# Kernel optimization log

Hardware: AMD Instinct MI355X
Metric: run time of the kernel (lower is better)

The kernel has to match this reference:

```python
import jax, jax.numpy as jnp
import numpy as np

N, D, H, DH, DFF, E = 4096, 512, 8, 64, 2048, 65536


def setup_inputs() -> dict:
    key = jax.random.key(0)
    ks = jax.random.split(key, 20)
    g = lambda k, s: jax.random.normal(k, s, dtype=jnp.float32) * 0.02
    inp = {
        'x': jax.random.normal(ks[0], (N, D), dtype=jnp.float32),
        'edge_index': jax.random.randint(ks[1], (2, E), 0, N),
        'edge_attr': jax.random.uniform(ks[2], (E,), dtype=jnp.float32),
        'Wg': g(ks[3], (D, D)), 'bg': jnp.zeros((D,), jnp.float32),
        'ln1_s': jnp.ones((D,), jnp.float32), 'ln1_b': jnp.zeros((D,), jnp.float32),
        'Wq': g(ks[4], (D, D)), 'bq': jnp.zeros((D,), jnp.float32),
        'Wk': g(ks[5], (D, D)), 'bk': jnp.zeros((D,), jnp.float32),
        'Wv': g(ks[6], (D, D)), 'bv': jnp.zeros((D,), jnp.float32),
        'Wo': g(ks[7], (D, D)), 'bo': jnp.zeros((D,), jnp.float32),
        'ln2_s': jnp.ones((D,), jnp.float32), 'ln2_b': jnp.zeros((D,), jnp.float32),
        'W1': g(ks[8], (D, DFF)), 'b1': jnp.zeros((DFF,), jnp.float32),
        'W2': g(ks[9], (DFF, D)), 'b2': jnp.zeros((D,), jnp.float32),
        'Wa': g(ks[10], (2 * D, D)), 'ba': jnp.zeros((D,), jnp.float32),
    }
    return inp


def _ln(x, s, b):
    m = x.mean(-1, keepdims=True)
    v = ((x - m) ** 2).mean(-1, keepdims=True)
    return (x - m) * jax.lax.rsqrt(v + 1e-5) * s + b


def _gcn(x, edge_index, ew, Wg, bg):
    # GCNConv: linear, add self-loops (weight 1), sym deg normalization, scatter-add
    xt = x @ Wg                                   # [N, D]
    src = jnp.concatenate([edge_index[0], jnp.arange(N)])
    dst = jnp.concatenate([edge_index[1], jnp.arange(N)])
    w = jnp.concatenate([ew, jnp.ones((N,), ew.dtype)])
    deg = jax.ops.segment_sum(w, dst, num_segments=N)
    dinv = jnp.where(deg > 0, jax.lax.rsqrt(jnp.maximum(deg, 1e-12)), 0.0)
    coef = dinv[src] * w * dinv[dst]              # [E+N]
    out = jax.ops.segment_sum(xt[src] * coef[:, None], dst, num_segments=N)
    return out + bg


def _tfm(x, p):
    # pre-LN vanilla transformer block over all N nodes as one sequence
    h = _ln(x, p['ln1_s'], p['ln1_b'])
    q = (h @ p['Wq'] + p['bq']).reshape(N, H, DH)
    k = (h @ p['Wk'] + p['bk']).reshape(N, H, DH)
    v = (h @ p['Wv'] + p['bv']).reshape(N, H, DH)
    scores = jnp.einsum('nhd,mhd->hnm', q, k) / np.sqrt(DH)
    a = jax.nn.softmax(scores, axis=-1)
    o = jnp.einsum('hnm,mhd->nhd', a, v).reshape(N, D)
    x = x + o @ p['Wo'] + p['bo']
    h2 = _ln(x, p['ln2_s'], p['ln2_b'])
    mlp = jax.nn.gelu(h2 @ p['W1'] + p['b1']) @ p['W2'] + p['b2']
    return x + mlp


def reference(x, edge_index, edge_attr, Wg, bg, ln1_s, ln1_b, Wq, bq, Wk, bk, Wv, bv,
              Wo, bo, ln2_s, ln2_b, W1, b1, W2, b2, Wa, ba):
    p = dict(ln1_s=ln1_s, ln1_b=ln1_b, Wq=Wq, bq=bq, Wk=Wk, bk=bk, Wv=Wv, bv=bv,
             Wo=Wo, bo=bo, ln2_s=ln2_s, ln2_b=ln2_b, W1=W1, b1=b1, W2=W2, b2=b2)
    mp = _gcn(x, edge_index, edge_attr, Wg, bg)
    tf = _tfm(x, p)
    return x + jnp.concatenate([mp, tf], axis=-1) @ Wa + ba
```

## Files before the change

### kernel.cpp

```cpp
#include <hip/hip_runtime.h>
#include <math.h>

#define N_NODES 4096
#define DMODEL  512
#define NHEAD   8
#define DHEAD   64
#define DFF     2048
#define NEDGE   65536
#define QKVLD   1536

typedef unsigned short u16;
typedef __bf16 bf16x8 __attribute__((ext_vector_type(8)));
typedef float  f32x4  __attribute__((ext_vector_type(4)));
typedef short  s16x4  __attribute__((ext_vector_type(4)));

#if defined(__has_builtin)
#if __has_builtin(__builtin_amdgcn_mfma_f32_16x16x16bf16_1k)
#define HAS_MFMA_1K 1
#endif
#endif

__device__ inline f32x4 mfma16(bf16x8 a, bf16x8 b, f32x4 c) {
    return __builtin_amdgcn_mfma_f32_16x16x32_bf16(a, b, c, 0, 0, 0);
}

#ifdef HAS_MFMA_1K
__device__ inline f32x4 mfma1k(s16x4 a, s16x4 b, f32x4 c) {
    return __builtin_amdgcn_mfma_f32_16x16x16bf16_1k(a, b, c, 0, 0, 0);
}
__device__ inline s16x4 pack_bf4(f32x4 p) {
    union { float f; unsigned u; } a0, a1, a2, a3;
    a0.f = p[0]; a1.f = p[1]; a2.f = p[2]; a3.f = p[3];
    unsigned lo = __builtin_amdgcn_perm(a1.u + 0x8000u, a0.u + 0x8000u, 0x07060302u);
    unsigned hi = __builtin_amdgcn_perm(a3.u + 0x8000u, a2.u + 0x8000u, 0x07060302u);
    union { unsigned u[2]; s16x4 v; } r;
    r.u[0] = lo; r.u[1] = hi;
    return r.v;
}
#endif

__device__ inline u16 f2bf(float f) {
    union { float f; unsigned u; } v; v.f = f;
    unsigned r = v.u + 0x7fff + ((v.u >> 16) & 1);
    return (u16)(r >> 16);
}

__device__ inline float bf2f(u16 v) {
    union { unsigned u; float f; } t; t.u = ((unsigned)v) << 16; return t.f;
}

__device__ inline float gelu_tanh(float x) {
    float x3 = x * x * x;
    float t = tanhf(0.7978845608028654f * (x + 0.044715f * x3));
    return 0.5f * x * (1.0f + t);
}

#define GBM 128
#define GBN 128
#define GBK 32
#define GP  40

template <int ACT, int OBF16>
__launch_bounds__(256)
__global__ void mfma_gemm(const u16* __restrict__ A, const u16* __restrict__ Bt,
                          const float* __restrict__ bias, const float* __restrict__ res,
                          void* __restrict__ Cout, int M, int Nn, int K, float scale,
                          int ldC, int ldRes) {
    __shared__ u16 Asm[2][GBM * GP];
    __shared__ u16 Bsm[2][GBN * GP];

    const int tid = threadIdx.x;
    const int w = tid >> 6;
    const int lane = tid & 63;
    const int quad = lane >> 4;
    const int l15 = lane & 15;
    const int row0 = blockIdx.y * GBM;
    const int col0 = blockIdx.x * GBN;
    const int wm = (w & 1) * 64;
    const int wn = (w >> 1) * 64;

    f32x4 acc[4][4];
#pragma unroll
    for (int i = 0; i < 4; ++i)
#pragma unroll
        for (int j = 0; j < 4; ++j) acc[i][j] = (f32x4){0.f, 0.f, 0.f, 0.f};

    const int c1 = tid, c2 = tid + 256;
    const int ar1 = c1 >> 2, ak1 = (c1 & 3) * 8;
    const int ar2 = c2 >> 2, ak2 = (c2 & 3) * 8;

    {
        uint4 a0 = *(const uint4*)&A [(size_t)(row0 + ar1) * K + ak1];
        uint4 a1 = *(const uint4*)&A [(size_t)(row0 + ar2) * K + ak2];
        uint4 b0 = *(const uint4*)&Bt[(size_t)(col0 + ar1) * K + ak1];
        uint4 b1 = *(const uint4*)&Bt[(size_t)(col0 + ar2) * K + ak2];
        *(uint4*)&Asm[0][ar1 * GP + ak1] = a0;
        *(uint4*)&Asm[0][ar2 * GP + ak2] = a1;
        *(uint4*)&Bsm[0][ar1 * GP + ak1] = b0;
        *(uint4*)&Bsm[0][ar2 * GP + ak2] = b1;
    }
    __syncthreads();

    const int nT = K / GBK;
    for (int t = 0; t < nT; ++t) {
        const int buf = t & 1;
        uint4 an0, an1, bn0, bn1;
        if (t + 1 < nT) {
            const int k0 = (t + 1) * GBK;
            an0 = *(const uint4*)&A [(size_t)(row0 + ar1) * K + k0 + ak1];
            an1 = *(const uint4*)&A [(size_t)(row0 + ar2) * K + k0 + ak2];
            bn0 = *(const uint4*)&Bt[(size_t)(col0 + ar1) * K + k0 + ak1];
            bn1 = *(const uint4*)&Bt[(size_t)(col0 + ar2) * K + k0 + ak2];
        }
        bf16x8 af[4], bf[4];
#pragma unroll
        for (int i = 0; i < 4; ++i) {
            af[i] = *(const bf16x8*)&Asm[buf][(wm + i * 16 + l15) * GP + quad * 8];
            bf[i] = *(const bf16x8*)&Bsm[buf][(wn + i * 16 + l15) * GP + quad * 8];
        }
#pragma unroll
        for (int i = 0; i < 4; ++i)
#pragma unroll
            for (int j = 0; j < 4; ++j)
                acc[i][j] = mfma16(af[i], bf[j], acc[i][j]);
        if (t + 1 < nT) {
            *(uint4*)&Asm[buf ^ 1][ar1 * GP + ak1] = an0;
            *(uint4*)&Asm[buf ^ 1][ar2 * GP + ak2] = an1;
            *(uint4*)&Bsm[buf ^ 1][ar1 * GP + ak1] = bn0;
            *(uint4*)&Bsm[buf ^ 1][ar2 * GP + ak2] = bn1;
            __syncthreads();
        }
    }

#pragma unroll
    for (int j = 0; j < 4; ++j) {
        const int col = col0 + wn + j * 16 + l15;
        const float bc = bias ? bias[col] : 0.f;
#pragma unroll
        for (int i = 0; i < 4; ++i) {
#pragma unroll
            for (int r = 0; r < 4; ++r) {
                const int row = row0 + wm + i * 16 + quad * 4 + r;
                float o = (acc[i][j][r] + bc) * scale;
                if (ACT == 1) o = gelu_tanh(o);
                if (res) o += res[(size_t)row * ldRes + col];
                if (OBF16)
                    ((u16*)Cout)[(size_t)row * ldC + col] = f2bf(o);
                else
                    ((float*)Cout)[(size_t)row * ldC + col] = o;
            }
        }
    }
}

template <int ACT, int OBF16>
__launch_bounds__(256)
__global__ void mfma_gemm64(const u16* __restrict__ A, const u16* __restrict__ Bt,
                            const float* __restrict__ bias, const float* __restrict__ res,
                            void* __restrict__ Cout, int M, int Nn, int K, float scale,
                            int ldC, int ldRes) {
    __shared__ u16 Asm[2][64 * GP];
    __shared__ u16 Bsm[2][128 * GP];

    const int tid = threadIdx.x;
    const int w = tid >> 6;
    const int lane = tid & 63;
    const int quad = lane >> 4;
    const int l15 = lane & 15;
    const int row0 = blockIdx.y * 64;
    const int col0 = blockIdx.x * GBN;
    const int wn = w * 32;

    f32x4 acc[4][2];
#pragma unroll
    for (int i = 0; i < 4; ++i)
#pragma unroll
        for (int j = 0; j < 2; ++j) acc[i][j] = (f32x4){0.f, 0.f, 0.f, 0.f};

    const int c1 = tid, c2 = tid + 256;
    const int ar1 = c1 >> 2, ak1 = (c1 & 3) * 8;
    const int ar2 = c2 >> 2, ak2 = (c2 & 3) * 8;

    {
        uint4 a0 = *(const uint4*)&A [(size_t)(row0 + ar1) * K + ak1];
        uint4 b0 = *(const uint4*)&Bt[(size_t)(col0 + ar1) * K + ak1];
        uint4 b1 = *(const uint4*)&Bt[(size_t)(col0 + ar2) * K + ak2];
        *(uint4*)&Asm[0][ar1 * GP + ak1] = a0;
        *(uint4*)&Bsm[0][ar1 * GP + ak1] = b0;
        *(uint4*)&Bsm[0][ar2 * GP + ak2] = b1;
    }
    __syncthreads();

    const int nT = K / GBK;
    for (int t = 0; t < nT; ++t) {
        const int buf = t & 1;
        uint4 an, bn0, bn1;
        if (t + 1 < nT) {
            const int k0 = (t + 1) * GBK;
            an  = *(const uint4*)&A [(size_t)(row0 + ar1) * K + k0 + ak1];
            bn0 = *(const uint4*)&Bt[(size_t)(col0 + ar1) * K + k0 + ak1];
            bn1 = *(const uint4*)&Bt[(size_t)(col0 + ar2) * K + k0 + ak2];
        }
        bf16x8 af[4], bf[2];
#pragma unroll
        for (int i = 0; i < 4; ++i)
            af[i] = *(const bf16x8*)&Asm[buf][(i * 16 + l15) * GP + quad * 8];
#pragma unroll
        for (int j = 0; j < 2; ++j)
            bf[j] = *(const bf16x8*)&Bsm[buf][(wn + j * 16 + l15) * GP + quad * 8];
#pragma unroll
        for (int i = 0; i < 4; ++i)
#pragma unroll
            for (int j = 0; j < 2; ++j)
                acc[i][j] = mfma16(af[i], bf[j], acc[i][j]);
        if (t + 1 < nT) {
            *(uint4*)&Asm[buf ^ 1][ar1 * GP + ak1] = an;
            *(uint4*)&Bsm[buf ^ 1][ar1 * GP + ak1] = bn0;
            *(uint4*)&Bsm[buf ^ 1][ar2 * GP + ak2] = bn1;
            __syncthreads();
        }
    }

#pragma unroll
    for (int j = 0; j < 2; ++j) {
        const int col = col0 + wn + j * 16 + l15;
        const float bc = bias ? bias[col] : 0.f;
#pragma unroll
        for (int i = 0; i < 4; ++i) {
#pragma unroll
            for (int r = 0; r < 4; ++r) {
                const int row = row0 + i * 16 + quad * 4 + r;
                float o = (acc[i][j][r] + bc) * scale;
                if (ACT == 1) o = gelu_tanh(o);
                if (res) o += res[(size_t)row * ldRes + col];
                if (OBF16)
                    ((u16*)Cout)[(size_t)row * ldC + col] = f2bf(o);
                else
                    ((float*)Cout)[(size_t)row * ldC + col] = o;
            }
        }
    }
}

__launch_bounds__(256)
__global__ void qkvg_gemm(const u16* __restrict__ xb, const u16* __restrict__ hb,
                          const u16* __restrict__ Wall,
                          const float* __restrict__ bq, const float* __restrict__ bk,
                          const float* __restrict__ bv,
                          u16* __restrict__ xtb, u16* __restrict__ qkvb) {
    __shared__ u16 Asm[2][64 * GP];
    __shared__ u16 Bsm[2][128 * GP];

    const int tid = threadIdx.x;
    const int w = tid >> 6;
    const int lane = tid & 63;
    const int quad = lane >> 4;
    const int l15 = lane & 15;
    const int row0 = blockIdx.y * 64;
    const int col0 = blockIdx.x * GBN;
    const int wn = w * 32;
    const int K = DMODEL;
    const u16* A = (col0 < 512) ? xb : hb;

    f32x4 acc[4][2];
#pragma unroll
    for (int i = 0; i < 4; ++i)
#pragma unroll
        for (int j = 0; j < 2; ++j) acc[i][j] = (f32x4){0.f, 0.f, 0.f, 0.f};

    const int c1 = tid, c2 = tid + 256;
    const int ar1 = c1 >> 2, ak1 = (c1 & 3) * 8;
    const int ar2 = c2 >> 2, ak2 = (c2 & 3) * 8;

    {
        uint4 a0 = *(const uint4*)&A   [(size_t)(row0 + ar1) * K + ak1];
        uint4 b0 = *(const uint4*)&Wall[(size_t)(col0 + ar1) * K + ak1];
        uint4 b1 = *(const uint4*)&Wall[(size_t)(col0 + ar2) * K + ak2];
        *(uint4*)&Asm[0][ar1 * GP + ak1] = a0;
        *(uint4*)&Bsm[0][ar1 * GP + ak1] = b0;
        *(uint4*)&Bsm[0][ar2 * GP + ak2] = b1;
    }
    __syncthreads();

    const int nT = K / GBK;
    for (int t = 0; t < nT; ++t) {
        const int buf = t & 1;
        uint4 an, bn0, bn1;
        if (t + 1 < nT) {
            const int k0 = (t + 1) * GBK;
            an  = *(const uint4*)&A   [(size_t)(row0 + ar1) * K + k0 + ak1];
            bn0 = *(const uint4*)&Wall[(size_t)(col0 + ar1) * K + k0 + ak1];
            bn1 = *(const uint4*)&Wall[(size_t)(col0 + ar2) * K + k0 + ak2];
        }
        bf16x8 af[4], bf[2];
#pragma unroll
        for (int i = 0; i < 4; ++i)
            af[i] = *(const bf16x8*)&Asm[buf][(i * 16 + l15) * GP + quad * 8];
#pragma unroll
        for (int j = 0; j < 2; ++j)
            bf[j] = *(const bf16x8*)&Bsm[buf][(wn + j * 16 + l15) * GP + quad * 8];
#pragma unroll
        for (int i = 0; i < 4; ++i)
#pragma unroll
            for (int j = 0; j < 2; ++j)
                acc[i][j] = mfma16(af[i], bf[j], acc[i][j]);
        if (t + 1 < nT) {
            *(uint4*)&Asm[buf ^ 1][ar1 * GP + ak1] = an;
            *(uint4*)&Bsm[buf ^ 1][ar1 * GP + ak1] = bn0;
            *(uint4*)&Bsm[buf ^ 1][ar2 * GP + ak2] = bn1;
            __syncthreads();
        }
    }

#pragma unroll
    for (int j = 0; j < 2; ++j) {
        const int col = col0 + wn + j * 16 + l15;
        float bc = 0.f, scale = 1.f;
        if (col >= 512 && col < 1024) { bc = bq[col - 512]; scale = 0.125f; }
        else if (col >= 1024 && col < 1536) bc = bk[col - 1024];
        else if (col >= 1536) bc = bv[col - 1536];
#pragma unroll
        for (int i = 0; i < 4; ++i) {
#pragma unroll
            for (int r = 0; r < 4; ++r) {
                const int row = row0 + i * 16 + quad * 4 + r;
                const u16 ob = f2bf((acc[i][j][r] + bc) * scale);
                if (col < 512)
                    xtb[(size_t)row * 512 + col] = ob;
                else
                    qkvb[(size_t)row * QKVLD + col - 512] = ob;
            }
        }
    }
}

__launch_bounds__(256)
__global__ void wtrans_all_kernel(
    const float* __restrict__ Wg, const float* __restrict__ Wq,
    const float* __restrict__ Wk, const float* __restrict__ Wv,
    const float* __restrict__ Wo, const float* __restrict__ W1,
    const float* __restrict__ W2, const float* __restrict__ Wa,
    u16* __restrict__ Wgt, u16* __restrict__ Wqt, u16* __restrict__ Wkt,
    u16* __restrict__ Wvt, u16* __restrict__ Wot, u16* __restrict__ W1t,
    u16* __restrict__ W2t, u16* __restrict__ Wat) {
    __shared__ u16 t[32][34];
    const int id = blockIdx.x;
    const float* W; u16* Wt; int K, Nn, bx, by;
    if (id < 1280) {
        const int m = id >> 8, tt = id & 255;
        bx = tt & 15; by = tt >> 4; K = 512; Nn = 512;
        W  = (m == 0) ? Wg  : (m == 1) ? Wq  : (m == 2) ? Wk  : (m == 3) ? Wv  : Wo;
        Wt = (m == 0) ? Wgt : (m == 1) ? Wqt : (m == 2) ? Wkt : (m == 3) ? Wvt : Wot;
    } else if (id < 2304) {
        const int tt = id - 1280; bx = tt & 63; by = tt >> 6;
        K = 512; Nn = 2048; W = W1; Wt = W1t;
    } else if (id < 3328) {
        const int tt = id - 2304; bx = tt & 15; by = tt >> 4;
        K = 2048; Nn = 512; W = W2; Wt = W2t;
    } else {
        const int tt = id - 3328; bx = tt & 15; by = tt >> 4;
        K = 1024; Nn = 512; W = Wa; Wt = Wat;
    }
    const int k0 = by * 32, n0 = bx * 32;
    const int r = threadIdx.x >> 3, c4 = (threadIdx.x & 7) * 4;
    float4 v = *(const float4*)&W[(size_t)(k0 + r) * Nn + n0 + c4];
    t[r][c4 + 0] = f2bf(v.x); t[r][c4 + 1] = f2bf(v.y);
    t[r][c4 + 2] = f2bf(v.z); t[r][c4 + 3] = f2bf(v.w);
    __syncthreads();
    u16 tmp[4];
#pragma unroll
    for (int i = 0; i < 4; ++i) tmp[i] = t[c4 + i][r];
    u16* op = Wt + (size_t)(n0 + r) * K + k0 + c4;
    *(uint2*)op = *(uint2*)tmp;
}

__global__ void cvt_bf16_kernel(const float* __restrict__ in, u16* __restrict__ out) {
    size_t i = ((size_t)blockIdx.x * 256 + threadIdx.x) * 4;
    float4 v = *(const float4*)&in[i];
    ushort4 o;
    o.x = f2bf(v.x); o.y = f2bf(v.y); o.z = f2bf(v.z); o.w = f2bf(v.w);
    *(ushort4*)&out[i] = o;
}

__device__ inline float block_sum_256(float v, float* red4) {
#pragma unroll
    for (int o = 32; o > 0; o >>= 1) v += __shfl_down(v, o, 64);
    const int lane = threadIdx.x & 63;
    const int w = threadIdx.x >> 6;
    if (lane == 0) red4[w] = v;
    __syncthreads();
    return red4[0] + red4[1] + red4[2] + red4[3];
}

__launch_bounds__(256)
__global__ void ln_kernel(const float* __restrict__ X, const float* __restrict__ s,
                          const float* __restrict__ b, u16* __restrict__ Y) {
    __shared__ float redA[4];
    __shared__ float redB[4];
    const int row = blockIdx.x;
    const int tid = threadIdx.x;
    const float* xr = X + (size_t)row * DMODEL;
    float v0 = xr[tid], v1 = xr[tid + 256];
    float total = block_sum_256(v0 + v1, redA);
    float mean = total * (1.0f / DMODEL);
    float d0 = v0 - mean, d1 = v1 - mean;
    float sq = block_sum_256(d0 * d0 + d1 * d1, redB);
    float inv = rsqrtf(sq * (1.0f / DMODEL) + 1e-5f);
    Y[(size_t)row * DMODEL + tid] = f2bf(d0 * inv * s[tid] + b[tid]);
    Y[(size_t)row * DMODEL + tid + 256] = f2bf(d1 * inv * s[tid + 256] + b[tid + 256]);
}

__global__ void gcn_prep_kernel(float* __restrict__ deg, int* __restrict__ cnt) {
    int i = blockIdx.x * 256 + threadIdx.x;
    deg[i] = 1.0f;
    cnt[i] = 0;
}

__global__ void gcn_count_kernel(const int* __restrict__ ei, const float* __restrict__ ew,
                                 float* __restrict__ deg, int* __restrict__ cnt) {
    int e = blockIdx.x * 256 + threadIdx.x;
    int d = ei[NEDGE + e];
    atomicAdd(&cnt[d], 1);
    atomicAdd(&deg[d], ew[e]);
}

__global__ void dinv_kernel(const float* __restrict__ deg, float* __restrict__ dinv) {
    int i = blockIdx.x * 256 + threadIdx.x;
    float d = deg[i];
    dinv[i] = (d > 0.f) ? rsqrtf(fmaxf(d, 1e-12f)) : 0.f;
}

__launch_bounds__(256)
__global__ void gcn_prefix_kernel(const int* __restrict__ cnt, int* __restrict__ off,
                                  int* __restrict__ cur) {
    __shared__ int part[256];
    const int tid = threadIdx.x;
    int local[16];
    int s = 0;
#pragma unroll
    for (int i = 0; i < 16; ++i) { local[i] = s; s += cnt[tid * 16 + i]; }
    part[tid] = s;
    __syncthreads();
    if (tid == 0) {
        int run = 0;
        for (int j = 0; j < 256; ++j) { int t = part[j]; part[j] = run; run += t; }
        off[N_NODES] = run;
    }
    __syncthreads();
    int p = part[tid];
#pragma unroll
    for (int i = 0; i < 16; ++i) {
        off[tid * 16 + i] = p + local[i];
        cur[tid * 16 + i] = p + local[i];
    }
}

__global__ void gcn_fill_kernel(const int* __restrict__ ei, const float* __restrict__ ew,
                                int* __restrict__ cur, int* __restrict__ esrc,
                                float* __restrict__ eww) {
    int e = blockIdx.x * 256 + threadIdx.x;
    int s = ei[e], d = ei[NEDGE + e];
    int pos = atomicAdd(&cur[d], 1);
    esrc[pos] = s;
    eww[pos] = ew[e];
}

__launch_bounds__(256)
__global__ void gcn_gather_kernel(const u16* __restrict__ xtb, const int* __restrict__ off,
                                  const int* __restrict__ esrc, const float* __restrict__ eww,
                                  const float* __restrict__ dinv, const float* __restrict__ bg,
                                  u16* __restrict__ catb) {
    const int d = blockIdx.x;
    const int b0 = off[d], b1 = off[d + 1];
    const float did = dinv[d];
    const int c = threadIdx.x * 2;
    float a0 = 0.f, a1 = 0.f;
    for (int j = b0; j < b1; ++j) {
        const int s = esrc[j];
        const float coef = dinv[s] * eww[j] * did;
        const unsigned pv = *(const unsigned*)&xtb[(size_t)s * DMODEL + c];
        a0 += coef * bf2f((u16)(pv & 0xffff));
        a1 += coef * bf2f((u16)(pv >> 16));
    }
    {
        const unsigned pv = *(const unsigned*)&xtb[(size_t)d * DMODEL + c];
        const float sl = did * did;
        a0 += sl * bf2f((u16)(pv & 0xffff));
        a1 += sl * bf2f((u16)(pv >> 16));
    }
    const unsigned pk = (unsigned)f2bf(a0 + bg[c]) | ((unsigned)f2bf(a1 + bg[c + 1]) << 16);
    *(unsigned*)&catb[(size_t)d * 1024 + c] = pk;
}

__launch_bounds__(256)
__global__ void vtrans_kernel(const u16* __restrict__ Qkv, u16* __restrict__ Vt) {
    __shared__ u16 t[64][72];
    const int h = blockIdx.x, n0 = blockIdx.y * 64;
    const int r = threadIdx.x >> 2, cg = (threadIdx.x & 3) * 16;
    const uint4* vp = (const uint4*)(Qkv + (size_t)(n0 + r) * QKVLD + 1024 + h * DHEAD + cg);
    *(uint4*)&t[r][cg] = vp[0];
    *(uint4*)&t[r][cg + 8] = vp[1];
    __syncthreads();
    const int d = threadIdx.x >> 2;
    u16 tmp[16];
#pragma unroll
    for (int i = 0; i < 16; ++i) tmp[i] = t[cg + i][d];
    u16* op = Vt + ((size_t)h * DHEAD + d) * N_NODES + n0 + cg;
    *(uint4*)&op[0] = *(uint4*)&tmp[0];
    *(uint4*)&op[8] = *(uint4*)&tmp[8];
}

#define TK 64
#define AP 88
#define NSPLIT 4
#define KSPAN (N_NODES / NSPLIT)

__launch_bounds__(128)
__global__ void attn_kernel(const u16* __restrict__ Qkv, const u16* __restrict__ Vtb,
                            float* __restrict__ Op0, float* __restrict__ Op1,
                            float* __restrict__ Op2, float* __restrict__ Op3,
                            float* __restrict__ lpart) {
    __shared__ u16 Ks[64 * AP];
    __shared__ u16 Vs[64 * AP];
#ifndef HAS_MFMA_1K
    __shared__ u16 Ps[2][2][16 * AP];
#endif

    const int h = blockIdx.x;
    const int q0 = blockIdx.y * 64;
    const int sp = blockIdx.z;
    float* __restrict__ Opx = (sp == 0) ? Op0 : (sp == 1) ? Op1 : (sp == 2) ? Op2 : Op3;
    const int kbase = sp * KSPAN;

    const int tid = threadIdx.x;
    const int w = tid >> 6;
    const int lane = tid & 63;
    const int quad = lane >> 4;
    const int l15 = lane & 15;

    const u16* qp = Qkv + (size_t)(q0 + w * 32 + l15) * QKVLD + h * DHEAD + quad * 8;
    bf16x8 qf[2][2];
    qf[0][0] = *(const bf16x8*)qp;
    qf[0][1] = *(const bf16x8*)(qp + 32);
    qf[1][0] = *(const bf16x8*)(qp + 16 * QKVLD);
    qf[1][1] = *(const bf16x8*)(qp + 16 * QKVLD + 32);

    f32x4 Oa[2][4];
#pragma unroll
    for (int a = 0; a < 2; ++a)
#pragma unroll
        for (int g = 0; g < 4; ++g) Oa[a][g] = (f32x4){0.f, 0.f, 0.f, 0.f};
    float ls[2] = {0.f, 0.f};

    const int sr = tid >> 1, sc = (tid & 1) * 32;

    for (int kt = kbase; kt < kbase + KSPAN; kt += TK) {
        {
            const uint4* kg = (const uint4*)(Qkv + (size_t)(kt + sr) * QKVLD + 512 + h * DHEAD + sc);
            uint4* kd = (uint4*)&Ks[sr * AP + sc];
            kd[0] = kg[0]; kd[1] = kg[1]; kd[2] = kg[2]; kd[3] = kg[3];
            const uint4* vg = (const uint4*)(Vtb + ((size_t)h * DHEAD + sr) * N_NODES + kt + sc);
            uint4* vd = (uint4*)&Vs[sr * AP + sc];
            vd[0] = vg[0]; vd[1] = vg[1]; vd[2] = vg[2]; vd[3] = vg[3];
        }
        __syncthreads();

        f32x4 St[2][4];
#pragma unroll
        for (int f = 0; f < 4; ++f) {
            const u16* kr = &Ks[(f * 16 + l15) * AP + quad * 8];
            bf16x8 k0 = *(const bf16x8*)kr;
            bf16x8 k1 = *(const bf16x8*)(kr + 32);
#pragma unroll
            for (int a = 0; a < 2; ++a) {
                f32x4 z = (f32x4){0.f, 0.f, 0.f, 0.f};
                z = mfma16(k0, qf[a][0], z);
                St[a][f] = mfma16(k1, qf[a][1], z);
            }
        }

#ifdef HAS_MFMA_1K
        s16x4 pk[2][4];
#pragma unroll
        for (int a = 0; a < 2; ++a)
#pragma unroll
            for (int f = 0; f < 4; ++f) {
                f32x4 p;
                p[0] = __expf(St[a][f][0]);
                p[1] = __expf(St[a][f][1]);
                p[2] = __expf(St[a][f][2]);
                p[3] = __expf(St[a][f][3]);
                ls[a] += (p[0] + p[1]) + (p[2] + p[3]);
                pk[a][f] = pack_bf4(p);
            }
#pragma unroll
        for (int f = 0; f < 4; ++f)
#pragma unroll
            for (int g = 0; g < 4; ++g) {
                const s16x4 vv = *(const s16x4*)&Vs[(g * 16 + l15) * AP + f * 16 + quad * 4];
                Oa[0][g] = mfma1k(pk[0][f], vv, Oa[0][g]);
                Oa[1][g] = mfma1k(pk[1][f], vv, Oa[1][g]);
            }
#else
        bf16x8 pa[2][2];
#pragma unroll
        for (int a = 0; a < 2; ++a) {
            u16* pw = Ps[w][a];
#pragma unroll
            for (int f = 0; f < 4; ++f) {
                float p0 = __expf(St[a][f][0]);
                float p1 = __expf(St[a][f][1]);
                float p2 = __expf(St[a][f][2]);
                float p3 = __expf(St[a][f][3]);
                ls[a] += (p0 + p1) + (p2 + p3);
                ushort4 pkk;
                pkk.x = f2bf(p0); pkk.y = f2bf(p1); pkk.z = f2bf(p2); pkk.w = f2bf(p3);
                *(uint2*)&pw[l15 * AP + f * 16 + quad * 4] = *(uint2*)&pkk;
            }
            const u16* pr = &pw[l15 * AP + quad * 8];
            pa[a][0] = *(const bf16x8*)pr;
            pa[a][1] = *(const bf16x8*)(pr + 32);
        }
#pragma unroll
        for (int g = 0; g < 4; ++g) {
            const u16* vr = &Vs[(g * 16 + l15) * AP + quad * 8];
            bf16x8 v0 = *(const bf16x8*)vr;
            bf16x8 v1 = *(const bf16x8*)(vr + 32);
#pragma unroll
            for (int a = 0; a < 2; ++a) {
                Oa[a][g] = mfma16(pa[a][0], v0, Oa[a][g]);
                Oa[a][g] = mfma16(pa[a][1], v1, Oa[a][g]);
            }
        }
#endif
        __syncthreads();
    }

#pragma unroll
    for (int a = 0; a < 2; ++a) {
        float s = ls[a];
        s += __shfl_xor(s, 16, 64);
        s += __shfl_xor(s, 32, 64);
        const int rowbase = q0 + w * 32 + a * 16;
        if (quad == 0)
            lpart[(size_t)(sp * NHEAD + h) * N_NODES + rowbase + l15] = s;
#pragma unroll
        for (int r = 0; r < 4; ++r) {
            float* op = Opx + (size_t)(rowbase + quad * 4 + r) * DMODEL + h * DHEAD + l15;
#pragma unroll
            for (int g = 0; g < 4; ++g) op[g * 16] = Oa[a][g][r];
        }
    }
}

__global__ void attn_reduce_kernel(const float* __restrict__ Op0, const float* __restrict__ Op1,
                                   const float* __restrict__ Op2, const float* __restrict__ Op3,
                                   const float* __restrict__ lpart, u16* __restrict__ attb) {
    size_t i4 = ((size_t)blockIdx.x * 256 + threadIdx.x) * 4;
    const int row = (int)(i4 >> 9);
    const int h = ((int)i4 & 511) >> 6;
    float4 o0 = *(const float4*)&Op0[i4];
    float4 o1 = *(const float4*)&Op1[i4];
    float4 o2 = *(const float4*)&Op2[i4];
    float4 o3 = *(const float4*)&Op3[i4];
    const float* lp = lpart + (size_t)h * N_NODES + row;
    const size_t S = (size_t)NHEAD * N_NODES;
    float inv = 1.0f / (lp[0] + lp[S] + lp[2 * S] + lp[3 * S]);
    ushort4 r;
    r.x = f2bf((o0.x + o1.x + o2.x + o3.x) * inv);
    r.y = f2bf((o0.y + o1.y + o2.y + o3.y) * inv);
    r.z = f2bf((o0.z + o1.z + o2.z + o3.z) * inv);
    r.w = f2bf((o0.w + o1.w + o2.w + o3.w) * inv);
    *(ushort4*)&attb[i4] = r;
}

static void mgemm(hipStream_t st, const u16* A, const u16* Bt, const float* bias,
                  const float* res, void* C, int M, int Nn, int K, float scale,
                  int act, int obf16, int ldC, int ldRes) {
    dim3 g(Nn / GBN, M / GBM), b(256);
    if (act)
        hipLaunchKernelGGL((mfma_gemm<1, 1>), g, b, 0, st, A, Bt, bias, res, C, M, Nn, K, scale, ldC, ldRes);
    else if (obf16)
        hipLaunchKernelGGL((mfma_gemm<0, 1>), g, b, 0, st, A, Bt, bias, res, C, M, Nn, K, scale, ldC, ldRes);
    else
        hipLaunchKernelGGL((mfma_gemm<0, 0>), g, b, 0, st, A, Bt, bias, res, C, M, Nn, K, scale, ldC, ldRes);
}

static void mgemm64(hipStream_t st, const u16* A, const u16* Bt, const float* bias,
                    const float* res, void* C, int M, int Nn, int K, float scale,
                    int act, int obf16, int ldC, int ldRes) {
    dim3 g(Nn / GBN, M / 64), b(256);
    if (act)
        hipLaunchKernelGGL((mfma_gemm64<1, 1>), g, b, 0, st, A, Bt, bias, res, C, M, Nn, K, scale, ldC, ldRes);
    else if (obf16)
        hipLaunchKernelGGL((mfma_gemm64<0, 1>), g, b, 0, st, A, Bt, bias, res, C, M, Nn, K, scale, ldC, ldRes);
    else
        hipLaunchKernelGGL((mfma_gemm64<0, 0>), g, b, 0, st, A, Bt, bias, res, C, M, Nn, K, scale, ldC, ldRes);
}

extern "C" void kernel_launch(void* const* d_in, const int* in_sizes, int n_in,
                              void* d_out, int out_size, void* d_ws, size_t ws_size,
                              hipStream_t stream) {
    const float* x    = (const float*)d_in[0];
    const int*   ei   = (const int*)d_in[1];
    const float* ew   = (const float*)d_in[2];
    const float* Wg   = (const float*)d_in[3];
    const float* bg   = (const float*)d_in[4];
    const float* ln1s = (const float*)d_in[5];
    const float* ln1b = (const float*)d_in[6];
    const float* Wq   = (const float*)d_in[7];
    const float* bq   = (const float*)d_in[8];
    const float* Wk   = (const float*)d_in[9];
    const float* bk   = (const float*)d_in[10];
    const float* Wv   = (const float*)d_in[11];
    const float* bv   = (const float*)d_in[12];
    const float* Wo   = (const float*)d_in[13];
    const float* bo   = (const float*)d_in[14];
    const float* ln2s = (const float*)d_in[15];
    const float* ln2b = (const float*)d_in[16];
    const float* W1   = (const float*)d_in[17];
    const float* b1   = (const float*)d_in[18];
    const float* W2   = (const float*)d_in[19];
    const float* b2   = (const float*)d_in[20];
    const float* Wa   = (const float*)d_in[21];
    const float* ba   = (const float*)d_in[22];
    float* out = (float*)d_out;
    float* ws  = (float*)d_ws;

    const size_t SLOT = (size_t)N_NODES * DMODEL;

    u16*   xtb = (u16*)ws;
    float* Op2 = ws;
    float* x1  = ws;
    float* lpart = ws + SLOT;
    int*   esrc  = (int*)(ws + SLOT + 262144);
    float* eww   = (float*)(esrc + NEDGE);
    int*   off   = (int*)(eww + NEDGE);
    int*   cur   = off + 4100;
    int*   cnt   = cur + 4096;
    float* Op3 = ws + 2 * SLOT;
    u16* hb   = (u16*)(ws + 3 * SLOT);
    u16* attb = hb + SLOT;
    u16* h2b  = hb + SLOT;
    u16* qkvb = (u16*)(ws + 4 * SLOT);
    u16* vtb  = (u16*)(ws + 5 * SLOT) + SLOT;
    float* Op0  = ws + 6 * SLOT;
    float* Op1  = ws + 7 * SLOT;
    u16*   midb = (u16*)(ws + 6 * SLOT);
    u16* catb = (u16*)(ws + 8 * SLOT);
    u16* xb   = catb;
    u16* Wgt = (u16*)(ws + 9 * SLOT);
    u16* Wqt = Wgt + 262144;
    u16* Wkt = Wqt + 262144;
    u16* Wvt = Wkt + 262144;
    u16* Wot = Wvt + 262144;
    u16* W1t = Wot + 262144;
    u16* W2t = W1t + 1048576;
    u16* Wat = W2t + 1048576;
    float* deg  = (float*)(Wat + 524288);
    float* dinv = deg + N_NODES;

    hipLaunchKernelGGL(wtrans_all_kernel, dim3(3840), dim3(256), 0, stream,
                       Wg, Wq, Wk, Wv, Wo, W1, W2, Wa,
                       Wgt, Wqt, Wkt, Wvt, Wot, W1t, W2t, Wat);
    hipLaunchKernelGGL(cvt_bf16_kernel, dim3((int)(SLOT / 1024)), dim3(256), 0, stream, x, xb);
    hipLaunchKernelGGL(ln_kernel, dim3(N_NODES), dim3(256), 0, stream, x, ln1s, ln1b, hb);

    hipLaunchKernelGGL(qkvg_gemm, dim3(16, 64), dim3(256), 0, stream,
                       xb, hb, Wgt, bq, bk, bv, xtb, qkvb);

    hipLaunchKernelGGL(gcn_prep_kernel, dim3(N_NODES / 256), dim3(256), 0, stream, deg, cnt);
    hipLaunchKernelGGL(gcn_count_kernel, dim3(NEDGE / 256), dim3(256), 0, stream, ei, ew, deg, cnt);
    hipLaunchKernelGGL(dinv_kernel, dim3(N_NODES / 256), dim3(256), 0, stream, deg, dinv);
    hipLaunchKernelGGL(gcn_prefix_kernel, dim3(1), dim3(256), 0, stream, cnt, off, cur);
    hipLaunchKernelGGL(gcn_fill_kernel, dim3(NEDGE / 256), dim3(256), 0, stream, ei, ew, cur, esrc, eww);
    hipLaunchKernelGGL(gcn_gather_kernel, dim3(N_NODES), dim3(256), 0, stream,
                       xtb, off, esrc, eww, dinv, bg, catb);

    hipLaunchKernelGGL(vtrans_kernel, dim3(NHEAD, N_NODES / 64), dim3(256), 0, stream, qkvb, vtb);
    hipLaunchKernelGGL(attn_kernel, dim3(NHEAD, N_NODES / 64, NSPLIT), dim3(128), 0, stream,
                       qkvb, vtb, Op0, Op1, Op2, Op3, lpart);
    hipLaunchKernelGGL(attn_reduce_kernel, dim3((int)(SLOT / 1024)), dim3(256), 0, stream,
                       Op0, Op1, Op2, Op3, lpart, attb);

    mgemm64(stream, attb, Wot, bo, x, x1, N_NODES, DMODEL, DMODEL, 1.0f, 0, 0, DMODEL, DMODEL);
    hipLaunchKernelGGL(ln_kernel, dim3(N_NODES), dim3(256), 0, stream, x1, ln2s, ln2b, h2b);
    mgemm(stream, h2b, W1t, b1, nullptr, midb, N_NODES, DFF, DMODEL, 1.0f, 1, 1, DFF, DFF);
    mgemm64(stream, midb, W2t, b2, x1, catb + 512, N_NODES, DMODEL, DFF, 1.0f, 0, 1, 1024, DMODEL);

    mgemm64(stream, catb, Wat, ba, x, out, N_NODES, DMODEL, 2 * DMODEL, 1.0f, 0, 0, DMODEL, DMODEL);
}
```

Baseline: 380.8 us.

## Fuse prep kernels, write V transposed from QKV GEMM, widen gemm64 to 512 threads

Merges the weight transpose, x-to-bf16 conversion, LN1 and GCN degree/count initialisation into one prep launch, and folds the dinv computation into the prefix kernel. The QKV GEMM epilogue now writes V directly in transposed layout, which removes the separate vtrans kernel. The 64-row GEMM moves to 512 threads with a 2x4 warp grid, so each warp holds a smaller accumulator tile. Together these cut launch count and extra passes over memory. The cost is a heterogeneous prep kernel whose blocks do uneven work, and strided 8-byte stores for the transposed V.

```diff
diff --git a/kernel.cpp b/kernel.cpp
--- a/kernel.cpp
+++ b/kernel.cpp
@@ -154,7 +154,7 @@
 }
 
 template <int ACT, int OBF16>
-__launch_bounds__(256)
+__launch_bounds__(512)
 __global__ void mfma_gemm64(const u16* __restrict__ A, const u16* __restrict__ Bt,
                             const float* __restrict__ bias, const float* __restrict__ res,
                             void* __restrict__ Cout, int M, int Nn, int K, float scale,
@@ -169,67 +169,66 @@
     const int l15 = lane & 15;
     const int row0 = blockIdx.y * 64;
     const int col0 = blockIdx.x * GBN;
-    const int wn = w * 32;
-
-    f32x4 acc[4][2];
-#pragma unroll
-    for (int i = 0; i < 4; ++i)
+    const int rh = (w & 1) * 32;
+    const int cg = (w >> 1) * 32;
+
+    f32x4 acc[2][2];
+#pragma unroll
+    for (int i = 0; i < 2; ++i)
 #pragma unroll
         for (int j = 0; j < 2; ++j) acc[i][j] = (f32x4){0.f, 0.f, 0.f, 0.f};
 
-    const int c1 = tid, c2 = tid + 256;
-    const int ar1 = c1 >> 2, ak1 = (c1 & 3) * 8;
-    const int ar2 = c2 >> 2, ak2 = (c2 & 3) * 8;
+    const int brow = tid >> 2, bk = (tid & 3) * 8;
+    const int arow = (tid & 255) >> 2, ak = (tid & 3) * 8;
+    const bool doA = (tid < 256);
 
     {
-        uint4 a0 = *(const uint4*)&A [(size_t)(row0 + ar1) * K + ak1];
-        uint4 b0 = *(const uint4*)&Bt[(size_t)(col0 + ar1) * K + ak1];
-        uint4 b1 = *(const uint4*)&Bt[(size_t)(col0 + ar2) * K + ak2];
-        *(uint4*)&Asm[0][ar1 * GP + ak1] = a0;
-        *(uint4*)&Bsm[0][ar1 * GP + ak1] = b0;
-        *(uint4*)&Bsm[0][ar2 * GP + ak2] = b1;
+        uint4 b0 = *(const uint4*)&Bt[(size_t)(col0 + brow) * K + bk];
+        *(uint4*)&Bsm[0][brow * GP + bk] = b0;
+        if (doA) {
+            uint4 a0 = *(const uint4*)&A[(size_t)(row0 + arow) * K + ak];
+            *(uint4*)&Asm[0][arow * GP + ak] = a0;
+        }
     }
     __syncthreads();
 
     const int nT = K / GBK;
     for (int t = 0; t < nT; ++t) {
         const int buf = t & 1;
-        uint4 an, bn0, bn1;
+        uint4 an, bn;
         if (t + 1 < nT) {
             const int k0 = (t + 1) * GBK;
-            an  = *(const uint4*)&A [(size_t)(row0 + ar1) * K + k0 + ak1];
-            bn0 = *(const uint4*)&Bt[(size_t)(col0 + ar1) * K + k0 + ak1];
-            bn1 = *(const uint4*)&Bt[(size_t)(col0 + ar2) * K + k0 + ak2];
-        }
-        bf16x8 af[4], bf[2];
-#pragma unroll
-        for (int i = 0; i < 4; ++i)
-            af[i] = *(const bf16x8*)&Asm[buf][(i * 16 + l15) * GP + quad * 8];
+            bn = *(const uint4*)&Bt[(size_t)(col0 + brow) * K + k0 + bk];
+            if (doA) an = *(const uint4*)&A[(size_t)(row0 + arow) * K + k0 + ak];
+        }
+        bf16x8 af[2], bf[2];
+#pragma unroll
+        for (int i = 0; i < 2; ++i)
+            af[i] = *(const bf16x8*)&Asm[buf][(rh + i * 16 + l15) * GP + quad * 8];
 #pragma unroll
         for (int j = 0; j < 2; ++j)
-            bf[j] = *(const bf16x8*)&Bsm[buf][(wn + j * 16 + l15) * GP + quad * 8];
-#pragma unroll
-        for (int i = 0; i < 4; ++i)
+            bf[j] = *(const bf16x8*)&Bsm[buf][(cg + j * 16 + l15) * GP + quad * 8];
+#pragma unroll
+        for (int i = 0; i < 2; ++i)
 #pragma unroll
             for (int j = 0; j < 2; ++j)
                 acc[i][j] = mfma16(af[i], bf[j], acc[i][j]);
         if (t + 1 < nT) {
-            *(uint4*)&Asm[buf ^ 1][ar1 * GP + ak1] = an;
-            *(uint4*)&Bsm[buf ^ 1][ar1 * GP + ak1] = bn0;
-            *(uint4*)&Bsm[buf ^ 1][ar2 * GP + ak2] = bn1;
+            *(uint4*)&Bsm[buf ^ 1][brow * GP + bk] = bn;
+            if (doA) *(uint4*)&Asm[buf ^ 1][arow * GP + ak] = an;
             __syncthreads();
         }
     }
 
 #pragma unroll
     for (int j = 0; j < 2; ++j) {
-        const int col = col0 + wn + j * 16 + l15;
+        const int col = col0 + cg + j * 16 + l15;
         const float bc = bias ? bias[col] : 0.f;
 #pragma unroll
-        for (int i = 0; i < 4; ++i) {
+        for (int i = 0; i < 2; ++i) {
 #pragma unroll
             for (int r = 0; r < 4; ++r) {
-                const int row = row0 + i * 16 + quad * 4 + r;
+                const int row = row0 + rh + i * 16 + quad * 4 + r;
                 float o = (acc[i][j][r] + bc) * scale;
                 if (ACT == 1) o = gelu_tanh(o);
                 if (res) o += res[(size_t)row * ldRes + col];
@@ -247,7 +246,8 @@
                           const u16* __restrict__ Wall,
                           const float* __restrict__ bq, const float* __restrict__ bk,
                           const float* __restrict__ bv,
-                          u16* __restrict__ xtb, u16* __restrict__ qkvb) {
+                          u16* __restrict__ xtb, u16* __restrict__ qkvb,
+                          u16* __restrict__ vtb) {
     __shared__ u16 Asm[2][64 * GP];
     __shared__ u16 Bsm[2][128 * GP];
 
@@ -315,81 +315,118 @@
 #pragma unroll
     for (int j = 0; j < 2; ++j) {
         const int col = col0 + wn + j * 16 + l15;
-        float bc = 0.f, scale = 1.f;
-        if (col >= 512 && col < 1024) { bc = bq[col - 512]; scale = 0.125f; }
-        else if (col >= 1024 && col < 1536) bc = bk[col - 1024];
-        else if (col >= 1536) bc = bv[col - 1536];
-#pragma unroll
-        for (int i = 0; i < 4; ++i) {
-#pragma unroll
-            for (int r = 0; r < 4; ++r) {
-                const int row = row0 + i * 16 + quad * 4 + r;
-                const u16 ob = f2bf((acc[i][j][r] + bc) * scale);
-                if (col < 512)
-                    xtb[(size_t)row * 512 + col] = ob;
-                else
-                    qkvb[(size_t)row * QKVLD + col - 512] = ob;
+        if (col < 512) {
+#pragma unroll
+            for (int i = 0; i < 4; ++i)
+#pragma unroll
+                for (int r = 0; r < 4; ++r)
+                    xtb[(size_t)(row0 + i * 16 + quad * 4 + r) * 512 + col] =
+                        f2bf(acc[i][j][r]);
+        } else if (col < 1536) {
+            const float bc = (col < 1024) ? bq[col - 512] : bk[col - 1024];
+            const float scale = (col < 1024) ? 0.125f : 1.0f;
+#pragma unroll
+            for (int i = 0; i < 4; ++i)
+#pragma unroll
+                for (int r = 0; r < 4; ++r)
+                    qkvb[(size_t)(row0 + i * 16 + quad * 4 + r) * QKVLD + col - 512] =
+                        f2bf((acc[i][j][r] + bc) * scale);
+        } else {
+            const int hd = col - 1536;
+            const float bc = bv[hd];
+#pragma unroll
+            for (int i = 0; i < 4; ++i) {
+                ushort4 pk;
+                pk.x = f2bf(acc[i][j][0] + bc);
+                pk.y = f2bf(acc[i][j][1] + bc);
+                pk.z = f2bf(acc[i][j][2] + bc);
+                pk.w = f2bf(acc[i][j][3] + bc);
+                *(uint2*)&vtb[(size_t)hd * N_NODES + row0 + i * 16 + quad * 4] =
+                    *(uint2*)&pk;
             }
         }
     }
 }
 
+__device__ inline float block_sum_256(float v, float* red4) {
+#pragma unroll
+    for (int o = 32; o > 0; o >>= 1) v += __shfl_down(v, o, 64);
+    const int lane = threadIdx.x & 63;
+    const int w = threadIdx.x >> 6;
+    if (lane == 0) red4[w] = v;
+    __syncthreads();
+    return red4[0] + red4[1] + red4[2] + red4[3];
+}
+
 __launch_bounds__(256)
-__global__ void wtrans_all_kernel(
+__global__ void prep_kernel(
     const float* __restrict__ Wg, const float* __restrict__ Wq,
     const float* __restrict__ Wk, const float* __restrict__ Wv,
     const float* __restrict__ Wo, const float* __restrict__ W1,
     const float* __restrict__ W2, const float* __restrict__ Wa,
     u16* __restrict__ Wgt, u16* __restrict__ Wqt, u16* __restrict__ Wkt,
     u16* __restrict__ Wvt, u16* __restrict__ Wot, u16* __restrict__ W1t,
-    u16* __restrict__ W2t, u16* __restrict__ Wat) {
+    u16* __restrict__ W2t, u16* __restrict__ Wat,
+    const float* __restrict__ x, u16* __restrict__ xb,
+    const float* __restrict__ ln1s, const float* __restrict__ ln1b,
+    u16* __restrict__ hb, float* __restrict__ deg, int* __restrict__ cnt) {
     __shared__ u16 t[32][34];
+    __shared__ float redA[4];
+    __shared__ float redB[4];
     const int id = blockIdx.x;
-    const float* W; u16* Wt; int K, Nn, bx, by;
-    if (id < 1280) {
-        const int m = id >> 8, tt = id & 255;
-        bx = tt & 15; by = tt >> 4; K = 512; Nn = 512;
-        W  = (m == 0) ? Wg  : (m == 1) ? Wq  : (m == 2) ? Wk  : (m == 3) ? Wv  : Wo;
-        Wt = (m == 0) ? Wgt : (m == 1) ? Wqt : (m == 2) ? Wkt : (m == 3) ? Wvt : Wot;
-    } else if (id < 2304) {
-        const int tt = id - 1280; bx = tt & 63; by = tt >> 6;
-        K = 512; Nn = 2048; W = W1; Wt = W1t;
-    } else if (id < 3328) {
-        const int tt = id - 2304; bx = tt & 15; by = tt >> 4;
-        K = 2048; Nn = 512; W = W2; Wt = W2t;
+
+    if (id < 3840) {
+        const float* W; u16* Wt; int K, Nn, bx, by;
+        if (id < 1280) {
+            const int m = id >> 8, tt = id & 255;
+            bx = tt & 15; by = tt >> 4; K = 512; Nn = 512;
+            W  = (m == 0) ? Wg  : (m == 1) ? Wq  : (m == 2) ? Wk  : (m == 3) ? Wv  : Wo;
+            Wt = (m == 0) ? Wgt : (m == 1) ? Wqt : (m == 2) ? Wkt : (m == 3) ? Wvt : Wot;
+        } else if (id < 2304) {
+            const int tt = id - 1280; bx = tt & 63; by = tt >> 6;
+            K = 512; Nn = 2048; W = W1; Wt = W1t;
+        } else if (id < 3328) {
+            const int tt = id - 2304; bx = tt & 15; by = tt >> 4;
+            K = 2048; Nn = 512; W = W2; Wt = W2t;
+        } else {
+            const int tt = id - 3328; bx = tt & 15; by = tt >> 4;
+            K = 1024; Nn = 512; W = Wa; Wt = Wat;
+        }
+        const int k0 = by * 32, n0 = bx * 32;
+        const int r = threadIdx.x >> 3, c4 = (threadIdx.x & 7) * 4;
+        float4 v = *(const float4*)&W[(size_t)(k0 + r) * Nn + n0 + c4];
+        t[r][c4 + 0] = f2bf(v.x); t[r][c4 + 1] = f2bf(v.y);
+        t[r][c4 + 2] = f2bf(v.z); t[r][c4 + 3] = f2bf(v.w);
+        __syncthreads();
+        u16 tmp[4];
+#pragma unroll
+        for (int i = 0; i < 4; ++i) tmp[i] = t[c4 + i][r];
+        u16* op = Wt + (size_t)(n0 + r) * K + k0 + c4;
+        *(uint2*)op = *(uint2*)tmp;
+    } else if (id < 5888) {
+        size_t i = ((size_t)(id - 3840) * 256 + threadIdx.x) * 4;
+        float4 v = *(const float4*)&x[i];
+        ushort4 o;
+        o.x = f2bf(v.x); o.y = f2bf(v.y); o.z = f2bf(v.z); o.w = f2bf(v.w);
+        *(ushort4*)&xb[i] = o;
+    } else if (id < 9984) {
+        const int row = id - 5888;
+        const int tid = threadIdx.x;
+        const float* xr = x + (size_t)row * DMODEL;
+        float v0 = xr[tid], v1 = xr[tid + 256];
+        float total = block_sum_256(v0 + v1, redA);
+        float mean = total * (1.0f / DMODEL);
+        float d0 = v0 - mean, d1 = v1 - mean;
+        float sq = block_sum_256(d0 * d0 + d1 * d1, redB);
+        float inv = rsqrtf(sq * (1.0f / DMODEL) + 1e-5f);
+        hb[(size_t)row * DMODEL + tid] = f2bf(d0 * inv * ln1s[tid] + ln1b[tid]);
+        hb[(size_t)row * DMODEL + tid + 256] =
+            f2bf(d1 * inv * ln1s[tid + 256] + ln1b[tid + 256]);
     } else {
-        const int tt = id - 3328; bx = tt & 15; by = tt >> 4;
-        K = 1024; Nn = 512; W = Wa; Wt = Wat;
-    }
-    const int k0 = by * 32, n0 = bx * 32;
-    const int r = threadIdx.x >> 3, c4 = (threadIdx.x & 7) * 4;
-    float4 v = *(const float4*)&W[(size_t)(k0 + r) * Nn + n0 + c4];
-    t[r][c4 + 0] = f2bf(v.x); t[r][c4 + 1] = f2bf(v.y);
-    t[r][c4 + 2] = f2bf(v.z); t[r][c4 + 3] = f2bf(v.w);
-    __syncthreads();
-    u16 tmp[4];
-#pragma unroll
-    for (int i = 0; i < 4; ++i) tmp[i] = t[c4 + i][r];
-    u16* op = Wt + (size_t)(n0 + r) * K + k0 + c4;
-    *(uint2*)op = *(uint2*)tmp;
-}
-
-__global__ void cvt_bf16_kernel(const float* __restrict__ in, u16* __restrict__ out) {
-    size_t i = ((size_t)blockIdx.x * 256 + threadIdx.x) * 4;
-    float4 v = *(const float4*)&in[i];
-    ushort4 o;
-    o.x = f2bf(v.x); o.y = f2bf(v.y); o.z = f2bf(v.z); o.w = f2bf(v.w);
-    *(ushort4*)&out[i] = o;
-}
-
-__device__ inline float block_sum_256(float v, float* red4) {
-#pragma unroll
-    for (int o = 32; o > 0; o >>= 1) v += __shfl_down(v, o, 64);
-    const int lane = threadIdx.x & 63;
-    const int w = threadIdx.x >> 6;
-    if (lane == 0) red4[w] = v;
-    __syncthreads();
-    return red4[0] + red4[1] + red4[2] + red4[3];
+        int i = (id - 9984) * 256 + threadIdx.x;
+        deg[i] = 1.0f;
+        cnt[i] = 0;
+    }
 }
 
 __launch_bounds__(256)
@@ -410,12 +447,6 @@
     Y[(size_t)row * DMODEL + tid + 256] = f2bf(d1 * inv * s[tid + 256] + b[tid + 256]);
 }
 
-__global__ void gcn_prep_kernel(float* __restrict__ deg, int* __restrict__ cnt) {
-    int i = blockIdx.x * 256 + threadIdx.x;
-    deg[i] = 1.0f;
-    cnt[i] = 0;
-}
-
 __global__ void gcn_count_kernel(const int* __restrict__ ei, const float* __restrict__ ew,
                                  float* __restrict__ deg, int* __restrict__ cnt) {
     int e = blockIdx.x * 256 + threadIdx.x;
@@ -424,15 +455,10 @@
     atomicAdd(&deg[d], ew[e]);
 }
 
-__global__ void dinv_kernel(const float* __restrict__ deg, float* __restrict__ dinv) {
-    int i = blockIdx.x * 256 + threadIdx.x;
-    float d = deg[i];
-    dinv[i] = (d > 0.f) ? rsqrtf(fmaxf(d, 1e-12f)) : 0.f;
-}
-
 __launch_bounds__(256)
 __global__ void gcn_prefix_kernel(const int* __restrict__ cnt, int* __restrict__ off,
-                                  int* __restrict__ cur) {
+                                  int* __restrict__ cur, const float* __restrict__ deg,
+                                  float* __restrict__ dinv) {
     __shared__ int part[256];
     const int tid = threadIdx.x;
     int local[16];
@@ -440,6 +466,12 @@
 #pragma unroll
     for (int i = 0; i < 16; ++i) { local[i] = s; s += cnt[tid * 16 + i]; }
     part[tid] = s;
+#pragma unroll
+    for (int i = 0; i < 16; ++i) {
+        const int n = tid * 16 + i;
+        float d = deg[n];
+        dinv[n] = (d > 0.f) ? rsqrtf(fmaxf(d, 1e-12f)) : 0.f;
+    }
     __syncthreads();
     if (tid == 0) {
         int run = 0;
@@ -490,24 +522,6 @@
     }
     const unsigned pk = (unsigned)f2bf(a0 + bg[c]) | ((unsigned)f2bf(a1 + bg[c + 1]) << 16);
     *(unsigned*)&catb[(size_t)d * 1024 + c] = pk;
-}
-
-__launch_bounds__(256)
-__global__ void vtrans_kernel(const u16* __restrict__ Qkv, u16* __restrict__ Vt) {
-    __shared__ u16 t[64][72];
-    const int h = blockIdx.x, n0 = blockIdx.y * 64;
-    const int r = threadIdx.x >> 2, cg = (threadIdx.x & 3) * 16;
-    const uint4* vp = (const uint4*)(Qkv + (size_t)(n0 + r) * QKVLD + 1024 + h * DHEAD + cg);
-    *(uint4*)&t[r][cg] = vp[0];
-    *(uint4*)&t[r][cg + 8] = vp[1];
-    __syncthreads();
-    const int d = threadIdx.x >> 2;
-    u16 tmp[16];
-#pragma unroll
-    for (int i = 0; i < 16; ++i) tmp[i] = t[cg + i][d];
-    u16* op = Vt + ((size_t)h * DHEAD + d) * N_NODES + n0 + cg;
-    *(uint4*)&op[0] = *(uint4*)&tmp[0];
-    *(uint4*)&op[8] = *(uint4*)&tmp[8];
 }
 
 #define TK 64
@@ -689,7 +703,7 @@
 static void mgemm64(hipStream_t st, const u16* A, const u16* Bt, const float* bias,
                     const float* res, void* C, int M, int Nn, int K, float scale,
                     int act, int obf16, int ldC, int ldRes) {
-    dim3 g(Nn / GBN, M / 64), b(256);
+    dim3 g(Nn / GBN, M / 64), b(512);
     if (act)
         hipLaunchKernelGGL((mfma_gemm64<1, 1>), g, b, 0, st, A, Bt, bias, res, C, M, Nn, K, scale, ldC, ldRes);
     else if (obf16)
@@ -760,24 +774,20 @@
     float* deg  = (float*)(Wat + 524288);
     float* dinv = deg + N_NODES;
 
-    hipLaunchKernelGGL(wtrans_all_kernel, dim3(3840), dim3(256), 0, stream,
+    hipLaunchKernelGGL(prep_kernel, dim3(10000), dim3(256), 0, stream,
                        Wg, Wq, Wk, Wv, Wo, W1, W2, Wa,
-                       Wgt, Wqt, Wkt, Wvt, Wot, W1t, W2t, Wat);
-    hipLaunchKernelGGL(cvt_bf16_kernel, dim3((int)(SLOT / 1024)), dim3(256), 0, stream, x, xb);
-    hipLaunchKernelGGL(ln_kernel, dim3(N_NODES), dim3(256), 0, stream, x, ln1s, ln1b, hb);
+                       Wgt, Wqt, Wkt, Wvt, Wot, W1t, W2t, Wat,
+                       x, xb, ln1s, ln1b, hb, deg, cnt);
 
     hipLaunchKernelGGL(qkvg_gemm, dim3(16, 64), dim3(256), 0, stream,
-                       xb, hb, Wgt, bq, bk, bv, xtb, qkvb);
-
-    hipLaunchKernelGGL(gcn_prep_kernel, dim3(N_NODES / 256), dim3(256), 0, stream, deg, cnt);
+                       xb, hb, Wgt, bq, bk, bv, xtb, qkvb, vtb);
+
     hipLaunchKernelGGL(gcn_count_kernel, dim3(NEDGE / 256), dim3(256), 0, stream, ei, ew, deg, cnt);
-    hipLaunchKernelGGL(dinv_kernel, dim3(N_NODES / 256), dim3(256), 0, stream, deg, dinv);
-    hipLaunchKernelGGL(gcn_prefix_kernel, dim3(1), dim3(256), 0, stream, cnt, off, cur);
+    hipLaunchKernelGGL(gcn_prefix_kernel, dim3(1), dim3(256), 0, stream, cnt, off, cur, deg, dinv);
     hipLaunchKernelGGL(gcn_fill_kernel, dim3(NEDGE / 256), dim3(256), 0, stream, ei, ew, cur, esrc, eww);
     hipLaunchKernelGGL(gcn_gather_kernel, dim3(N_NODES), dim3(256), 0, stream,
                        xtb, off, esrc, eww, dinv, bg, catb);
 
-    hipLaunchKernelGGL(vtrans_kernel, dim3(NHEAD, N_NODES / 64), dim3(256), 0, stream, qkvb, vtb);
     hipLaunchKernelGGL(attn_kernel, dim3(NHEAD, N_NODES / 64, NSPLIT), dim3(128), 0, stream,
                        qkvb, vtb, Op0, Op1, Op2, Op3, lpart);
     hipLaunchKernelGGL(attn_reduce_kernel, dim3((int)(SLOT / 1024)), dim3(256), 0, stream,
```

Result: faster. 360.0 us (-5.5%).
